# Kernel tuning notes

Hardware: AMD Instinct MI355X
Metric: run time of the kernel (lower is better)

## Reference

```python
import jax, jax.numpy as jnp
import numpy as np

B, L, D, H, HID = 2048, 512, 17, 8, 256  # batch, max entities, feat dim, heads, mlp hidden
SPECIAL, OUT = 9, 23  # special vector dims, policy logits (7+16)


def _lin(k, out_d, in_d, scale):
    kw, kb = jax.random.split(k)
    W = jax.random.normal(kw, (out_d, in_d), jnp.float32) * scale
    b = jax.random.normal(kb, (out_d,), jnp.float32) * 0.01
    return W, b


def setup_inputs() -> dict:
    key = jax.random.key(0)
    ks = jax.random.split(key, 16)
    # observations: row 0 holds the 9-dim special vector, rows 1..L are ragged entities
    x = jax.random.normal(ks[0], (B, L + 1, D), jnp.float32)
    lengths = jax.random.randint(ks[1], (B,), 1, L + 1)
    mask = (jnp.arange(L)[None, :] < lengths[:, None]).astype(jnp.float32)
    x = x.at[:, 1:, :].multiply(mask[:, :, None])  # zero rows mark padding
    s = 1.0 / np.sqrt(D)
    # per-head K/V projections (num_heads separate tiny Linears)
    Wk = jax.random.normal(ks[2], (H, D, D), jnp.float32) * s
    bk = jax.random.normal(ks[3], (H, D), jnp.float32) * 0.01
    Wv = jax.random.normal(ks[4], (H, D, D), jnp.float32) * s
    bv = jax.random.normal(ks[5], (H, D), jnp.float32) * 0.01
    q = jax.random.normal(ks[6], (H, D), jnp.float32)  # learned per-head queries
    Wo, bo = _lin(ks[7], D, H * D, 1.0 / np.sqrt(H * D))
    sc = 1.0 / np.sqrt(D + SPECIAL)
    pW1, pb1 = _lin(ks[8], HID, D + SPECIAL, sc)
    pW2, pb2 = _lin(ks[9], HID, HID, 1.0 / np.sqrt(HID))
    pW3, pb3 = _lin(ks[10], OUT, HID, 1.0 / np.sqrt(HID))
    vW1, vb1 = _lin(ks[11], HID, D + SPECIAL, sc)
    vW2, vb2 = _lin(ks[12], HID, HID, 1.0 / np.sqrt(HID))
    vW3, vb3 = _lin(ks[13], 1, HID, 1.0 / np.sqrt(HID))
    return dict(x=x, Wk=Wk, bk=bk, Wv=Wv, bv=bv, q=q, Wo=Wo, bo=bo,
                pW1=pW1, pb1=pb1, pW2=pW2, pb2=pb2, pW3=pW3, pb3=pb3,
                vW1=vW1, vb1=vb1, vW2=vW2, vb2=vb2, vW3=vW3, vb3=vb3)


def _mlp(h, W1, b1, W2, b2, W3, b3):
    h = jax.nn.relu(h @ W1.T + b1)
    h = jax.nn.relu(h @ W2.T + b2)
    return h @ W3.T + b3


def reference(x, Wk, bk, Wv, bv, q, Wo, bo,
              pW1, pb1, pW2, pb2, pW3, pb3,
              vW1, vb1, vW2, vb2, vW3, vb3):
    special = x[:, 0, :SPECIAL]            # [B, 9]
    seq = x[:, 1:, :]                      # [B, L, D]
    mask = jnp.sum(jnp.abs(seq), axis=-1) != 0  # [B, L] non-padded rows
    # per-head keys/values for all samples at once (batched over the head loop)
    keys = jnp.einsum('bld,hed->bhle', seq, Wk) + bk[None, :, None, :]   # [B,H,L,D]
    vals = jnp.einsum('bld,hed->bhle', seq, Wv) + bv[None, :, None, :]   # [B,H,L,D]
    scores = jnp.einsum('bhle,he->bhl', keys, q)                          # [B,H,L]
    scores = jnp.where(mask[:, None, :], scores, -1e9)
    w = jax.nn.softmax(scores, axis=-1)                                   # [B,H,L]
    agg = jnp.einsum('bhl,bhle->bhe', w, vals).reshape(x.shape[0], H * D)  # concat heads
    attn = agg @ Wo.T + bo                                                # [B, D]
    comb = jnp.concatenate([attn, special], axis=-1)                      # [B, D+9]
    logits = _mlp(comb, pW1, pb1, pW2, pb2, pW3, pb3)                     # [B, 23]
    value = _mlp(comb, vW1, vb1, vW2, vb2, vW3, vb3)                      # [B, 1]
    return logits, value
```

## Files before the change

kernel.cpp:

```cpp
#include <hip/hip_runtime.h>
#include <hip/hip_bf16.h>

#define B_ 2048
#define D_ 17
#define H_ 8
#define HID_ 256
#define OUT_ 23
#define XROW 8721
#define SEQN 8704
#define LAST4 4465151

typedef unsigned int u32;
typedef const __attribute__((address_space(1))) u32* gp1_t;
typedef __attribute__((address_space(3))) u32* lp3_t;

__device__ __forceinline__ float bclane(float v, int l) {
  return __uint_as_float(__builtin_amdgcn_readlane(__float_as_uint(v), l));
}

__device__ __forceinline__ void gload_lds16(const float4* gsrc_lane, float* lds_wave_base) {
  __builtin_amdgcn_global_load_lds((gp1_t)(const void*)gsrc_lane,
                                   (lp3_t)(void*)lds_wave_base, 16, 0, 0);
}

__global__ __launch_bounds__(256) void prep_kernel(
    const float* __restrict__ pW2, const float* __restrict__ vW2,
    const float* __restrict__ Wk, const float* __restrict__ bk,
    const float* __restrict__ q,
    float* __restrict__ pW2t, float* __restrict__ vW2t, float* __restrict__ qkc)
{
  const int bid = blockIdx.x;
  const int t = threadIdx.x;
  if (bid == 128) {
    if (t < H_ * D_) {
      const int h = t / D_, dd = t - h * D_;
      float s = 0.f;
      #pragma unroll
      for (int e = 0; e < D_; ++e) s = fmaf(Wk[h*289 + e*D_ + dd], q[h*D_ + e], s);
      qkc[h*18 + dd] = s;
    } else if (t < H_ * D_ + H_) {
      const int h = t - H_ * D_;
      float s = 0.f;
      #pragma unroll
      for (int e = 0; e < D_; ++e) s = fmaf(bk[h*D_ + e], q[h*D_ + e], s);
      qkc[h*18 + 17] = s;
    }
    return;
  }
  __shared__ float tile[32][33];
  const int m = bid >> 6, tid = bid & 63;
  const int ti = (tid >> 3) * 32, tk = (tid & 7) * 32;
  const float* src = m ? vW2 : pW2;
  float* dst = m ? vW2t : pW2t;
  const int tx = t & 31, ty = t >> 5;
  #pragma unroll
  for (int r = 0; r < 4; ++r) tile[ty + 8*r][tx] = src[(ti + ty + 8*r)*HID_ + tk + tx];
  __syncthreads();
  #pragma unroll
  for (int r = 0; r < 4; ++r) dst[(tk + ty + 8*r)*HID_ + ti + tx] = tile[tx][ty + 8*r];
}

__global__ __launch_bounds__(256, 3) void fused_kernel(
    const float* __restrict__ x, const float* __restrict__ qkc,
    const float* __restrict__ Wv, const float* __restrict__ bv,
    const float* __restrict__ Wo, const float* __restrict__ bo,
    const float* __restrict__ pW1, const float* __restrict__ pb1,
    const float* __restrict__ pW2t, const float* __restrict__ pb2,
    const float* __restrict__ pW3, const float* __restrict__ pb3,
    const float* __restrict__ vW1, const float* __restrict__ vb1,
    const float* __restrict__ vW2t, const float* __restrict__ vb2,
    const float* __restrict__ vW3, const float* __restrict__ vb3,
    float* __restrict__ out)
{
  __shared__ __align__(16) float s_seq[9216];
  __shared__ float s_part[4][H_][18];
  __shared__ float s_swn[136];
  __shared__ float s_agg[136];
  __shared__ float s_wp[136];
  __shared__ float s_combL[4][28];

  const int t = threadIdx.x;
  const int w = t >> 6, lane = t & 63;
  const int hp = lane >> 4;
  const int rg = lane & 15;
  const float4* __restrict__ x4 = (const float4*)x;

  const float* q0 = qkc + (2*hp) * 18;
  float qk0[D_], qk1[D_];
  #pragma unroll
  for (int d = 0; d < D_; ++d) { qk0[d] = q0[d]; qk1[d] = q0[18 + d]; }
  const float ch0 = q0[17], ch1 = q0[35];

  #pragma unroll 1
  for (int j = 0; j < 4; ++j) {
    const int b = blockIdx.x * 4 + j;
    const int seq0 = b * XROW + D_;
    const int s4 = seq0 >> 2;
    const int phase = seq0 & 3;

    const float pv = x[seq0 + lane * 136];

    {
      float* dstb = s_seq + ((t & ~63) << 2);
      const int g0 = s4 + t;
      gload_lds16(x4 + g0,          dstb);
      gload_lds16(x4 + g0 + 256,    dstb + 1024);
      gload_lds16(x4 + g0 + 512,    dstb + 2048);
      gload_lds16(x4 + g0 + 768,    dstb + 3072);
      gload_lds16(x4 + g0 + 1024,   dstb + 4096);

      const unsigned long long live = __ballot(pv != 0.f) | 1ull;
      const int nr = 8 * (64 - __builtin_clzll(live));
      const int rounds = min(9, (nr * D_ + phase + 1023) >> 10);

      if (rounds > 5) gload_lds16(x4 + g0 + 1280, dstb + 5120);
      if (rounds > 6) gload_lds16(x4 + g0 + 1536, dstb + 6144);
      if (rounds > 7) gload_lds16(x4 + g0 + 1792, dstb + 7168);
      if (rounds > 8) gload_lds16(x4 + min(g0 + 2048, LAST4), dstb + 8192);
    }
    const unsigned long long live2 = __ballot(pv != 0.f) | 1ull;
    const int nrows = 8 * (64 - __builtin_clzll(live2));

    __syncthreads();

    float den0 = 0.f, den1 = 0.f;
    float acc0[D_], acc1[D_];
    #pragma unroll
    for (int d = 0; d < D_; ++d) { acc0[d] = 0.f; acc1[d] = 0.f; }

    auto dorow = [&](int row) {
      const float* rp = &s_seq[phase + row * D_];
      const float f0 = rp[0],  f1 = rp[1],  f2 = rp[2],  f3 = rp[3];
      const float f4 = rp[4],  f5 = rp[5],  f6 = rp[6],  f7 = rp[7];
      const float f8 = rp[8],  f9 = rp[9],  f10 = rp[10], f11 = rp[11];
      const float f12 = rp[12], f13 = rp[13], f14 = rp[14], f15 = rp[15];
      const float f16 = rp[16];
      float sA = ch0, sB = ch1;
      sA = fmaf(qk0[0],  f0,  sA); sB = fmaf(qk1[0],  f0,  sB);
      sA = fmaf(qk0[1],  f1,  sA); sB = fmaf(qk1[1],  f1,  sB);
      sA = fmaf(qk0[2],  f2,  sA); sB = fmaf(qk1[2],  f2,  sB);
      sA = fmaf(qk0[3],  f3,  sA); sB = fmaf(qk1[3],  f3,  sB);
      sA = fmaf(qk0[4],  f4,  sA); sB = fmaf(qk1[4],  f4,  sB);
      sA = fmaf(qk0[5],  f5,  sA); sB = fmaf(qk1[5],  f5,  sB);
      sA = fmaf(qk0[6],  f6,  sA); sB = fmaf(qk1[6],  f6,  sB);
      sA = fmaf(qk0[7],  f7,  sA); sB = fmaf(qk1[7],  f7,  sB);
      sA = fmaf(qk0[8],  f8,  sA); sB = fmaf(qk1[8],  f8,  sB);
      sA = fmaf(qk0[9],  f9,  sA); sB = fmaf(qk1[9],  f9,  sB);
      sA = fmaf(qk0[10], f10, sA); sB = fmaf(qk1[10], f10, sB);
      sA = fmaf(qk0[11], f11, sA); sB = fmaf(qk1[11], f11, sB);
      sA = fmaf(qk0[12], f12, sA); sB = fmaf(qk1[12], f12, sB);
      sA = fmaf(qk0[13], f13, sA); sB = fmaf(qk1[13], f13, sB);
      sA = fmaf(qk0[14], f14, sA); sB = fmaf(qk1[14], f14, sB);
      sA = fmaf(qk0[15], f15, sA); sB = fmaf(qk1[15], f15, sB);
      sA = fmaf(qk0[16], f16, sA); sB = fmaf(qk1[16], f16, sB);
      const bool lv = (row < nrows) && (f0 != 0.f);
      const float p0 = lv ? __expf(sA) : 0.f;
      const float p1 = lv ? __expf(sB) : 0.f;
      den0 += p0; den1 += p1;
      acc0[0]  = fmaf(p0, f0,  acc0[0]);  acc1[0]  = fmaf(p1, f0,  acc1[0]);
      acc0[1]  = fmaf(p0, f1,  acc0[1]);  acc1[1]  = fmaf(p1, f1,  acc1[1]);
      acc0[2]  = fmaf(p0, f2,  acc0[2]);  acc1[2]  = fmaf(p1, f2,  acc1[2]);
      acc0[3]  = fmaf(p0, f3,  acc0[3]);  acc1[3]  = fmaf(p1, f3,  acc1[3]);
      acc0[4]  = fmaf(p0, f4,  acc0[4]);  acc1[4]  = fmaf(p1, f4,  acc1[4]);
      acc0[5]  = fmaf(p0, f5,  acc0[5]);  acc1[5]  = fmaf(p1, f5,  acc1[5]);
      acc0[6]  = fmaf(p0, f6,  acc0[6]);  acc1[6]  = fmaf(p1, f6,  acc1[6]);
      acc0[7]  = fmaf(p0, f7,  acc0[7]);  acc1[7]  = fmaf(p1, f7,  acc1[7]);
      acc0[8]  = fmaf(p0, f8,  acc0[8]);  acc1[8]  = fmaf(p1, f8,  acc1[8]);
      acc0[9]  = fmaf(p0, f9,  acc0[9]);  acc1[9]  = fmaf(p1, f9,  acc1[9]);
      acc0[10] = fmaf(p0, f10, acc0[10]); acc1[10] = fmaf(p1, f10, acc1[10]);
      acc0[11] = fmaf(p0, f11, acc0[11]); acc1[11] = fmaf(p1, f11, acc1[11]);
      acc0[12] = fmaf(p0, f12, acc0[12]); acc1[12] = fmaf(p1, f12, acc1[12]);
      acc0[13] = fmaf(p0, f13, acc0[13]); acc1[13] = fmaf(p1, f13, acc1[13]);
      acc0[14] = fmaf(p0, f14, acc0[14]); acc1[14] = fmaf(p1, f14, acc1[14]);
      acc0[15] = fmaf(p0, f15, acc0[15]); acc1[15] = fmaf(p1, f15, acc1[15]);
      acc0[16] = fmaf(p0, f16, acc0[16]); acc1[16] = fmaf(p1, f16, acc1[16]);
    };

    {
      const int s0r = w * 64;
      if (s0r < nrows) {
        dorow(s0r + rg);
        dorow(s0r + rg + 16);
        dorow(s0r + rg + 32);
        dorow(s0r + rg + 48);
      }
      const int s1r = 256 + w * 64;
      if (s1r < nrows) {
        dorow(s1r + rg);
        dorow(s1r + rg + 16);
        dorow(s1r + rg + 32);
        dorow(s1r + rg + 48);
      }
    }

    #pragma unroll
    for (int m = 1; m <= 8; m <<= 1) {
      den0 += __shfl_xor(den0, m, 64);
      den1 += __shfl_xor(den1, m, 64);
      #pragma unroll
      for (int d = 0; d < D_; ++d) {
        acc0[d] += __shfl_xor(acc0[d], m, 64);
        acc1[d] += __shfl_xor(acc1[d], m, 64);
      }
    }
    if (rg == 0) {
      float* p0p = &s_part[w][2*hp][0];
      float* p1p = &s_part[w][2*hp + 1][0];
      p0p[0] = den0; p1p[0] = den1;
      #pragma unroll
      for (int d = 0; d < D_; ++d) { p0p[1 + d] = acc0[d]; p1p[1 + d] = acc1[d]; }
    }
    __syncthreads();

    if (t < 136) {
      const int hh = t / D_, d = t - hh * D_;
      float dn = 0.f, ac = 0.f;
      #pragma unroll
      for (int ww = 0; ww < 4; ++ww) { dn += s_part[ww][hh][0]; ac += s_part[ww][hh][1 + d]; }
      s_swn[t] = ac / dn;
    }
    __syncthreads();
    if (t < 136) {
      const int hh = t / D_, e = t - hh * D_;
      float s = bv[t];
      #pragma unroll
      for (int d = 0; d < D_; ++d) s = fmaf(Wv[hh*289 + e*D_ + d], s_swn[hh*D_ + d], s);
      s_agg[t] = s;
    }
    __syncthreads();
    if (t < 136) {
      const int o = t >> 3, pt = t & 7;
      float s = 0.f;
      #pragma unroll
      for (int jj = 0; jj < D_; ++jj) s = fmaf(Wo[o*136 + pt*D_ + jj], s_agg[pt*D_ + jj], s);
      s_wp[t] = s;
    }
    __syncthreads();
    if (t < D_) {
      float s = bo[t];
      #pragma unroll
      for (int pt = 0; pt < 8; ++pt) s += s_wp[t*8 + pt];
      s_combL[j][t] = s;
    } else if (t < 26) {
      s_combL[j][t] = x[b * XROW + (t - D_)];
    }
    __syncthreads();
  }

  float* s_red = s_seq;
  float* s_h2  = s_seq + 3072;
  const int kq = t >> 6, ln = t & 63;

  #pragma unroll
  for (int p = 0; p < 2; ++p) {
    const float* W1  = p ? vW1  : pW1;   const float* B1 = p ? vb1 : pb1;
    const float* W2t = p ? vW2t : pW2t;  const float* B2 = p ? vb2 : pb2;

    float h[4];
    {
      float a[4] = {0.f, 0.f, 0.f, 0.f};
      const float* wr = W1 + t * 26;
      for (int k = 0; k < 26; ++k) {
        const float wk = wr[k];
        #pragma unroll
        for (int bb = 0; bb < 4; ++bb) a[bb] = fmaf(wk, s_combL[bb][k], a[bb]);
      }
      const float bias = B1[t];
      #pragma unroll
      for (int bb = 0; bb < 4; ++bb) h[bb] = fmaxf(a[bb] + bias, 0.f);
    }

    float4 acc[4];
    #pragma unroll
    for (int bb = 0; bb < 4; ++bb) acc[bb] = make_float4(0.f, 0.f, 0.f, 0.f);
    {
      const float* wbase = W2t + (size_t)(kq * 64) * HID_ + 4 * ln;
      #pragma unroll 8
      for (int jj = 0; jj < 64; ++jj) {
        const float4 wv = *(const float4*)(wbase + (size_t)jj * HID_);
        #pragma unroll
        for (int bb = 0; bb < 4; ++bb) {
          const float hv = bclane(h[bb], jj);
          acc[bb].x = fmaf(wv.x, hv, acc[bb].x);
          acc[bb].y = fmaf(wv.y, hv, acc[bb].y);
          acc[bb].z = fmaf(wv.z, hv, acc[bb].z);
          acc[bb].w = fmaf(wv.w, hv, acc[bb].w);
        }
      }
    }
    if (kq > 0) {
      #pragma unroll
      for (int bb = 0; bb < 4; ++bb)
        *(float4*)&s_red[((kq - 1) * 4 + bb) * HID_ + 4 * ln] = acc[bb];
    }
    __syncthreads();
    if (kq == 0) {
      const float4 bias = *(const float4*)&B2[4 * ln];
      #pragma unroll
      for (int bb = 0; bb < 4; ++bb) {
        const float4 r0 = *(const float4*)&s_red[(0 * 4 + bb) * HID_ + 4 * ln];
        const float4 r1 = *(const float4*)&s_red[(1 * 4 + bb) * HID_ + 4 * ln];
        const float4 r2 = *(const float4*)&s_red[(2 * 4 + bb) * HID_ + 4 * ln];
        float4 rr;
        rr.x = fmaxf(acc[bb].x + r0.x + r1.x + r2.x + bias.x, 0.f);
        rr.y = fmaxf(acc[bb].y + r0.y + r1.y + r2.y + bias.y, 0.f);
        rr.z = fmaxf(acc[bb].z + r0.z + r1.z + r2.z + bias.z, 0.f);
        rr.w = fmaxf(acc[bb].w + r0.w + r1.w + r2.w + bias.w, 0.f);
        *(float4*)&s_h2[bb * HID_ + 4 * ln] = rr;
      }
    }
    __syncthreads();

    if (p == 0) {
      if (t < 92) {
        const int bb = t / OUT_, o = t - bb * OUT_;
        const float4* w4 = (const float4*)(pW3 + o * HID_);
        const float4* h4 = (const float4*)&s_h2[bb * HID_];
        float s = pb3[o];
        for (int k = 0; k < 64; ++k) {
          const float4 wv = w4[k], hv = h4[k];
          s = fmaf(wv.x, hv.x, fmaf(wv.y, hv.y, fmaf(wv.z, hv.z, fmaf(wv.w, hv.w, s))));
        }
        out[(size_t)(blockIdx.x * 4 + bb) * OUT_ + o] = s;
      }
    } else {
      if (t < 4) {
        const int bb = t;
        const float4* w4 = (const float4*)vW3;
        const float4* h4 = (const float4*)&s_h2[bb * HID_];
        float s = vb3[0];
        for (int k = 0; k < 64; ++k) {
          const float4 wv = w4[k], hv = h4[k];
          s = fmaf(wv.x, hv.x, fmaf(wv.y, hv.y, fmaf(wv.z, hv.z, fmaf(wv.w, hv.w, s))));
        }
        out[(size_t)B_ * OUT_ + blockIdx.x * 4 + bb] = s;
      }
    }
    __syncthreads();
  }
}

extern "C" void kernel_launch(void* const* d_in, const int* in_sizes, int n_in,
                              void* d_out, int out_size, void* d_ws, size_t ws_size,
                              hipStream_t stream) {
  (void)in_sizes; (void)n_in; (void)out_size; (void)ws_size;
  const float* x   = (const float*)d_in[0];
  const float* Wk  = (const float*)d_in[1];
  const float* bk  = (const float*)d_in[2];
  const float* Wv  = (const float*)d_in[3];
  const float* bv  = (const float*)d_in[4];
  const float* q   = (const float*)d_in[5];
  const float* Wo  = (const float*)d_in[6];
  const float* bo  = (const float*)d_in[7];
  const float* pW1 = (const float*)d_in[8];
  const float* pb1 = (const float*)d_in[9];
  const float* pW2 = (const float*)d_in[10];
  const float* pb2 = (const float*)d_in[11];
  const float* pW3 = (const float*)d_in[12];
  const float* pb3 = (const float*)d_in[13];
  const float* vW1 = (const float*)d_in[14];
  const float* vb1 = (const float*)d_in[15];
  const float* vW2 = (const float*)d_in[16];
  const float* vb2 = (const float*)d_in[17];
  const float* vW3 = (const float*)d_in[18];
  const float* vb3 = (const float*)d_in[19];
  float* out = (float*)d_out;

  float* pW2t = (float*)d_ws;
  float* vW2t = pW2t + (size_t)HID_ * HID_;
  float* qkc  = vW2t + (size_t)HID_ * HID_;

  prep_kernel<<<129, 256, 0, stream>>>(pW2, vW2, Wk, bk, q, pW2t, vW2t, qkc);
  fused_kernel<<<B_ / 4, 256, 0, stream>>>(x, qkc, Wv, bv, Wo, bo,
                                           pW1, pb1, pW2t, pb2, pW3, pb3,
                                           vW1, vb1, vW2t, vb2, vW3, vb3, out);
}
```

Measured before the change: 61.70 us.

## Split fused kernel into attention and MLP blocks linked by per-sample flags

Each fused block used to handle four samples in turn, running attention and then the MLP. Now one launch holds two block roles: 2048 attention blocks (one per sample) write the combined vector to global memory and set a flag, and 512 MLP blocks spin-wait on the flags of their four samples before running the policy and value MLPs. The aim is more parallelism in the attention phase and overlap of MLP work with attention work from other blocks. The cost is an extra kernel to zero the flags, global round trips for comb, and spin-waiting. Correctness relies on the attention blocks being scheduled before the MLP blocks that wait on them.

```diff
diff --git a/kernel.cpp b/kernel.cpp
--- a/kernel.cpp
+++ b/kernel.cpp
@@ -17,7 +17,6 @@
 __device__ __forceinline__ float bclane(float v, int l) {
   return __uint_as_float(__builtin_amdgcn_readlane(__float_as_uint(v), l));
 }
-
 __device__ __forceinline__ void gload_lds16(const float4* gsrc_lane, float* lds_wave_base) {
   __builtin_amdgcn_global_load_lds((gp1_t)(const void*)gsrc_lane,
                                    (lp3_t)(void*)lds_wave_base, 16, 0, 0);
@@ -60,7 +59,12 @@
   for (int r = 0; r < 4; ++r) dst[(tk + ty + 8*r)*HID_ + ti + tx] = tile[tx][ty + 8*r];
 }
 
-__global__ __launch_bounds__(256, 3) void fused_kernel(
+__global__ __launch_bounds__(512) void zeroflags_kernel(int* __restrict__ flags) {
+  const int i = blockIdx.x * 512 + threadIdx.x;
+  if (i < B_) flags[i] = 0;
+}
+
+__global__ __launch_bounds__(256, 3) void fused_pc_kernel(
     const float* __restrict__ x, const float* __restrict__ qkc,
     const float* __restrict__ Wv, const float* __restrict__ bv,
     const float* __restrict__ Wo, const float* __restrict__ bo,
@@ -70,33 +74,28 @@
     const float* __restrict__ vW1, const float* __restrict__ vb1,
     const float* __restrict__ vW2t, const float* __restrict__ vb2,
     const float* __restrict__ vW3, const float* __restrict__ vb3,
+    float* __restrict__ comb, int* __restrict__ flags,
     float* __restrict__ out)
 {
-  __shared__ __align__(16) float s_seq[9216];
-  __shared__ float s_part[4][H_][18];
-  __shared__ float s_swn[136];
-  __shared__ float s_agg[136];
-  __shared__ float s_wp[136];
-  __shared__ float s_combL[4][28];
-
+  __shared__ __align__(16) float smem[10200];
   const int t = threadIdx.x;
-  const int w = t >> 6, lane = t & 63;
-  const int hp = lane >> 4;
-  const int rg = lane & 15;
-  const float4* __restrict__ x4 = (const float4*)x;
-
-  const float* q0 = qkc + (2*hp) * 18;
-  float qk0[D_], qk1[D_];
-  #pragma unroll
-  for (int d = 0; d < D_; ++d) { qk0[d] = q0[d]; qk1[d] = q0[18 + d]; }
-  const float ch0 = q0[17], ch1 = q0[35];
-
-  #pragma unroll 1
-  for (int j = 0; j < 4; ++j) {
-    const int b = blockIdx.x * 4 + j;
+  const int bid = blockIdx.x;
+
+  if (bid < B_) {
+    float* s_seq = smem;
+    float* s_part = smem + 9216;
+    float* s_swn = smem + 9792;
+    float* s_agg = smem + 9928;
+    float* s_wp  = smem + 10064;
+
+    const int w = t >> 6, lane = t & 63;
+    const int hp = lane >> 4;
+    const int rg = lane & 15;
+    const int b = bid;
     const int seq0 = b * XROW + D_;
     const int s4 = seq0 >> 2;
     const int phase = seq0 & 3;
+    const float4* __restrict__ x4 = (const float4*)x;
 
     const float pv = x[seq0 + lane * 136];
 
@@ -120,6 +119,12 @@
     }
     const unsigned long long live2 = __ballot(pv != 0.f) | 1ull;
     const int nrows = 8 * (64 - __builtin_clzll(live2));
+
+    const float* q0 = qkc + (2*hp) * 18;
+    float qk0[D_], qk1[D_];
+    #pragma unroll
+    for (int d = 0; d < D_; ++d) { qk0[d] = q0[d]; qk1[d] = q0[18 + d]; }
+    const float ch0 = q0[17], ch1 = q0[35];
 
     __syncthreads();
 
@@ -179,17 +184,11 @@
     {
       const int s0r = w * 64;
       if (s0r < nrows) {
-        dorow(s0r + rg);
-        dorow(s0r + rg + 16);
-        dorow(s0r + rg + 32);
-        dorow(s0r + rg + 48);
+        dorow(s0r + rg); dorow(s0r + rg + 16); dorow(s0r + rg + 32); dorow(s0r + rg + 48);
       }
       const int s1r = 256 + w * 64;
       if (s1r < nrows) {
-        dorow(s1r + rg);
-        dorow(s1r + rg + 16);
-        dorow(s1r + rg + 32);
-        dorow(s1r + rg + 48);
+        dorow(s1r + rg); dorow(s1r + rg + 16); dorow(s1r + rg + 32); dorow(s1r + rg + 48);
       }
     }
 
@@ -204,8 +203,8 @@
       }
     }
     if (rg == 0) {
-      float* p0p = &s_part[w][2*hp][0];
-      float* p1p = &s_part[w][2*hp + 1][0];
+      float* p0p = &s_part[(w * H_ + 2*hp) * 18];
+      float* p1p = &s_part[(w * H_ + 2*hp + 1) * 18];
       p0p[0] = den0; p1p[0] = den1;
       #pragma unroll
       for (int d = 0; d < D_; ++d) { p0p[1 + d] = acc0[d]; p1p[1 + d] = acc1[d]; }
@@ -216,7 +215,10 @@
       const int hh = t / D_, d = t - hh * D_;
       float dn = 0.f, ac = 0.f;
       #pragma unroll
-      for (int ww = 0; ww < 4; ++ww) { dn += s_part[ww][hh][0]; ac += s_part[ww][hh][1 + d]; }
+      for (int ww = 0; ww < 4; ++ww) {
+        const float* pp = &s_part[(ww * H_ + hh) * 18];
+        dn += pp[0]; ac += pp[1 + d];
+      }
       s_swn[t] = ac / dn;
     }
     __syncthreads();
@@ -232,7 +234,7 @@
       const int o = t >> 3, pt = t & 7;
       float s = 0.f;
       #pragma unroll
-      for (int jj = 0; jj < D_; ++jj) s = fmaf(Wo[o*136 + pt*D_ + jj], s_agg[pt*D_ + jj], s);
+      for (int j = 0; j < D_; ++j) s = fmaf(Wo[o*136 + pt*D_ + j], s_agg[pt*D_ + j], s);
       s_wp[t] = s;
     }
     __syncthreads();
@@ -240,18 +242,40 @@
       float s = bo[t];
       #pragma unroll
       for (int pt = 0; pt < 8; ++pt) s += s_wp[t*8 + pt];
-      s_combL[j][t] = s;
+      comb[b*26 + t] = s;
     } else if (t < 26) {
-      s_combL[j][t] = x[b * XROW + (t - D_)];
-    }
-    __syncthreads();
+      comb[b*26 + t] = x[b * XROW + (t - D_)];
+    }
+    __syncthreads();
+    if (t == 0) {
+      __threadfence();
+      atomicExch(&flags[b], 1);
+    }
+    return;
   }
 
-  float* s_red = s_seq;
-  float* s_h2  = s_seq + 3072;
+  float* s_red  = smem;
+  float* s_h2   = smem + 3072;
+  float* s_comb = smem + 4096;
+
+  const int mid = bid - B_;
+  const int b0 = mid * 4;
+
+  if (t < 4) {
+    while (atomicAdd(&flags[b0 + t], 0) == 0) __builtin_amdgcn_s_sleep(16);
+  }
+  __syncthreads();
+  __threadfence();
+
+  if (t < 104) {
+    const int bb = t / 26, k = t - bb * 26;
+    s_comb[bb * 28 + k] = comb[(size_t)(b0 + bb) * 26 + k];
+  }
+  __syncthreads();
+
   const int kq = t >> 6, ln = t & 63;
 
-  #pragma unroll
+  #pragma unroll 1
   for (int p = 0; p < 2; ++p) {
     const float* W1  = p ? vW1  : pW1;   const float* B1 = p ? vb1 : pb1;
     const float* W2t = p ? vW2t : pW2t;  const float* B2 = p ? vb2 : pb2;
@@ -263,7 +287,7 @@
       for (int k = 0; k < 26; ++k) {
         const float wk = wr[k];
         #pragma unroll
-        for (int bb = 0; bb < 4; ++bb) a[bb] = fmaf(wk, s_combL[bb][k], a[bb]);
+        for (int bb = 0; bb < 4; ++bb) a[bb] = fmaf(wk, s_comb[bb * 28 + k], a[bb]);
       }
       const float bias = B1[t];
       #pragma unroll
@@ -321,7 +345,7 @@
           const float4 wv = w4[k], hv = h4[k];
           s = fmaf(wv.x, hv.x, fmaf(wv.y, hv.y, fmaf(wv.z, hv.z, fmaf(wv.w, hv.w, s))));
         }
-        out[(size_t)(blockIdx.x * 4 + bb) * OUT_ + o] = s;
+        out[(size_t)(b0 + bb) * OUT_ + o] = s;
       }
     } else {
       if (t < 4) {
@@ -333,7 +357,7 @@
           const float4 wv = w4[k], hv = h4[k];
           s = fmaf(wv.x, hv.x, fmaf(wv.y, hv.y, fmaf(wv.z, hv.z, fmaf(wv.w, hv.w, s))));
         }
-        out[(size_t)B_ * OUT_ + blockIdx.x * 4 + bb] = s;
+        out[(size_t)B_ * OUT_ + b0 + bb] = s;
       }
     }
     __syncthreads();
@@ -369,9 +393,13 @@
   float* pW2t = (float*)d_ws;
   float* vW2t = pW2t + (size_t)HID_ * HID_;
   float* qkc  = vW2t + (size_t)HID_ * HID_;
+  float* comb = qkc + 160;
+  int*   flags = (int*)(comb + (size_t)B_ * 26);
 
   prep_kernel<<<129, 256, 0, stream>>>(pW2, vW2, Wk, bk, q, pW2t, vW2t, qkc);
-  fused_kernel<<<B_ / 4, 256, 0, stream>>>(x, qkc, Wv, bv, Wo, bo,
-                                           pW1, pb1, pW2t, pb2, pW3, pb3,
-                                           vW1, vb1, vW2t, vb2, vW3, vb3, out);
-}
+  zeroflags_kernel<<<4, 512, 0, stream>>>(flags);
+  fused_pc_kernel<<<B_ + B_ / 4, 256, 0, stream>>>(x, qkc, Wv, bv, Wo, bo,
+                                                   pW1, pb1, pW2t, pb2, pW3, pb3,
+                                                   vW1, vb1, vW2t, vb2, vW3, vb3,
+                                                   comb, flags, out);
+}
```

After: 144.5 us. 2.34x slower.
